# Kernel optimization log

Measured on AMD Instinct MI355X. Metric: run time of the kernel, lower is better.

Reference implementation:

```python
import jax, jax.numpy as jnp
import numpy as np

B, C, H, W = 8, 512, 32, 32
MID = 64  # in_ch // k = 512 // 8
BN_EPS = 1e-5


def conv1x1(x, Wt, b):
    # x: [B,C,H,W], Wt: [O,C], b: [O]
    return jnp.einsum('bchw,oc->bohw', x, Wt) + b[None, :, None, None]


def batchnorm(x, gamma, beta):
    # train-mode BN: batch statistics over (B,H,W)
    mu = jnp.mean(x, axis=(0, 2, 3), keepdims=True)
    var = jnp.var(x, axis=(0, 2, 3), keepdims=True)
    xn = (x - mu) * jax.lax.rsqrt(var + BN_EPS)
    return xn * gamma[None, :, None, None] + beta[None, :, None, None]


def setup_inputs() -> dict:
    key = jax.random.key(0)
    ks = jax.random.split(key, 8)
    scale = 1.0 / np.sqrt(C)
    x = jax.random.normal(ks[0], (B, C, H, W), dtype=jnp.float32)
    Wf = jax.random.normal(ks[1], (MID, C), dtype=jnp.float32) * scale
    Wg = jax.random.normal(ks[2], (MID, C), dtype=jnp.float32) * scale
    Wh = jax.random.normal(ks[3], (MID, C), dtype=jnp.float32) * scale
    Wv = jax.random.normal(ks[4], (C, MID), dtype=jnp.float32) * (1.0 / np.sqrt(MID))
    return {
        'x': x,
        'Wf': Wf, 'bf': jnp.zeros((MID,), jnp.float32),
        'gamma_f': jnp.ones((MID,), jnp.float32), 'beta_f': jnp.zeros((MID,), jnp.float32),
        'Wg': Wg, 'bg': jnp.zeros((MID,), jnp.float32),
        'gamma_g': jnp.ones((MID,), jnp.float32), 'beta_g': jnp.zeros((MID,), jnp.float32),
        'Wh': Wh, 'bh': jnp.zeros((MID,), jnp.float32),
        'Wv': Wv, 'bv': jnp.zeros((C,), jnp.float32),
    }


def reference(x, Wf, bf, gamma_f, beta_f, Wg, bg, gamma_g, beta_g, Wh, bh, Wv, bv):
    b, c, h, w = x.shape
    hw = h * w
    f_x = jax.nn.relu(batchnorm(conv1x1(x, Wf, bf), gamma_f, beta_f)).reshape(b, MID, hw)
    g_x = jax.nn.relu(batchnorm(conv1x1(x, Wg, bg), gamma_g, beta_g)).reshape(b, MID, hw)
    h_x = conv1x1(x, Wh, bh).reshape(b, MID, hw)
    # z = f_x^T @ g_x : [B, HW, HW]
    z = jnp.einsum('bcn,bcm->bnm', f_x, g_x)
    # spectral normalization by the top singular value
    S = jnp.linalg.svd(z, compute_uv=False)  # sorted descending
    sigma = S[:, 0][:, None, None]
    attn = z / sigma
    # attn @ h_x^T -> [B, HW, MID], then permute to [B, MID, H, W]
    z2 = jnp.einsum('bnm,bcm->bcn', attn, h_x).reshape(b, MID, h, w)
    return conv1x1(z2, Wv, bv) + x
```

## Files before the change

### kernel.cpp

```cpp
#include <hip/hip_runtime.h>

#define B_   8
#define C_   512
#define HW_  1024
#define NCOL (B_*HW_)
#define NROWS 192
#define EPS  1e-5f
#define NCHUNK 32

#define YOFF   0
#define YSZ    (NROWS*NCOL)
#define SPOFF  (YOFF+YSZ)
#define SPSZ   256
#define WOFF   (SPOFF+SPSZ)
#define WSZ    98304
#define CPOFF  (WOFF+WSZ)
#define CPSZ   (24*NCHUNK*4096)
#define CMOFF  (CPOFF+CPSZ)
#define CMSZ   (24*4096)
#define ISOFF  (CMOFF+CMSZ)
#define UOFF   (ISOFF+16)

typedef unsigned short u16;
typedef __attribute__((ext_vector_type(8))) short short8;
typedef __attribute__((ext_vector_type(4))) float f32x4;

__device__ __forceinline__ u16 f2bf(float f) {
  unsigned u = __float_as_uint(f);
  unsigned r = u + 0x7fffu + ((u >> 16) & 1u);
  return (u16)(r >> 16);
}
__device__ __forceinline__ float bf2f(u16 h) {
  return __uint_as_float(((unsigned)h) << 16);
}
#define MFMA_B16(a,b,c) __builtin_amdgcn_mfma_f32_16x16x32_bf16(a,b,c,0,0,0)

#define FMA16(a, bb) \
  acc[0][0]+=a.x*bb.x; acc[0][1]+=a.x*bb.y; acc[0][2]+=a.x*bb.z; acc[0][3]+=a.x*bb.w; \
  acc[1][0]+=a.y*bb.x; acc[1][1]+=a.y*bb.y; acc[1][2]+=a.y*bb.z; acc[1][3]+=a.y*bb.w; \
  acc[2][0]+=a.z*bb.x; acc[2][1]+=a.z*bb.y; acc[2][2]+=a.z*bb.z; acc[2][3]+=a.z*bb.w; \
  acc[3][0]+=a.w*bb.x; acc[3][1]+=a.w*bb.y; acc[3][2]+=a.w*bb.z; acc[3][3]+=a.w*bb.w;

__global__ __launch_bounds__(256) void k_prep(
    const float* __restrict__ Wf, const float* __restrict__ Wg,
    const float* __restrict__ Wh, float* __restrict__ ws)
{
  u16* Whi = (u16*)(ws + WOFF);
  u16* Wlo = Whi + NROWS*C_;
  const int e4 = blockIdx.x*256 + threadIdx.x;
  const int e  = e4*4;
  const int row = e >> 9, k = e & 511;
  const float* src = (row < 64) ? &Wf[row*C_ + k]
                   : (row < 128) ? &Wg[(row-64)*C_ + k]
                   : &Wh[(row-128)*C_ + k];
  const float4 v = *reinterpret_cast<const float4*>(src);
  u16 h0=f2bf(v.x), h1=f2bf(v.y), h2=f2bf(v.z), h3=f2bf(v.w);
  u16 l0=f2bf(v.x-bf2f(h0)), l1=f2bf(v.y-bf2f(h1)), l2=f2bf(v.z-bf2f(h2)), l3=f2bf(v.w-bf2f(h3));
  uint2 ph; ph.x = (unsigned)h0 | ((unsigned)h1<<16); ph.y = (unsigned)h2 | ((unsigned)h3<<16);
  uint2 pl; pl.x = (unsigned)l0 | ((unsigned)l1<<16); pl.y = (unsigned)l2 | ((unsigned)l3<<16);
  *reinterpret_cast<uint2*>(&Whi[e]) = ph;
  *reinterpret_cast<uint2*>(&Wlo[e]) = pl;
}

__global__ __launch_bounds__(256) void k_conv(
    const float* __restrict__ x,
    const float* __restrict__ bf, const float* __restrict__ bg, const float* __restrict__ bh,
    float* __restrict__ ws)
{
  __shared__ u16 Xh[8*32*8];
  __shared__ u16 Xl[8*32*8];
  __shared__ u16 Swh[4][3][2][512];
  __shared__ u16 Swl[4][3][2][512];
  const u16* Whi = (const u16*)(ws + WOFF);
  const u16* Wlo = Whi + NROWS*C_;
  const int bid = blockIdx.x;
  const int n0  = bid * 32;
  const int b   = n0 >> 10;
  const int hw0 = n0 & 1023;
  const int t   = threadIdx.x;
  const int lane = t & 63;
  const int wid  = t >> 6;
  const int wrow0 = wid * 48;
  const int cst = t & 31, kg2 = t >> 5;
  const int lm = lane & 15, lk = lane >> 4;

  float xr[64];
  {
    const float* xp = x + ((size_t)(b*C_ + kg2*8))*HW_ + hw0 + cst;
    #pragma unroll
    for (int j = 0; j < 8; ++j)
      #pragma unroll
      for (int i = 0; i < 8; ++i)
        xr[j*8+i] = xp[(size_t)(j*64 + i)*HW_];
  }

  f32x4 acc[3][2];
  #pragma unroll
  for (int i=0;i<3;++i) { acc[i][0]=(f32x4)0.f; acc[i][1]=(f32x4)0.f; }

  #pragma unroll
  for (int j = 0; j < 8; ++j) {
    const int kk = j*64;
    __syncthreads();
    {
      uint4 th[6], tl[6];
      #pragma unroll
      for (int mt = 0; mt < 3; ++mt)
        #pragma unroll
        for (int kb = 0; kb < 2; ++kb) {
          const size_t widx = (size_t)(wrow0 + mt*16 + lm)*C_ + kk + kb*32 + lk*8;
          th[mt*2+kb] = *reinterpret_cast<const uint4*>(&Whi[widx]);
          tl[mt*2+kb] = *reinterpret_cast<const uint4*>(&Wlo[widx]);
        }
      #pragma unroll
      for (int mt = 0; mt < 3; ++mt)
        #pragma unroll
        for (int kb = 0; kb < 2; ++kb) {
          *reinterpret_cast<uint4*>(&Swh[wid][mt][kb][lane*8]) = th[mt*2+kb];
          *reinterpret_cast<uint4*>(&Swl[wid][mt][kb][lane*8]) = tl[mt*2+kb];
        }
    }
    {
      u16 hb[8], lb[8];
      #pragma unroll
      for (int i=0;i<8;++i) {
        const float v = xr[j*8+i];
        hb[i] = f2bf(v); lb[i] = f2bf(v - bf2f(hb[i]));
      }
      uint4 ph, pl;
      ph.x=(unsigned)hb[0]|((unsigned)hb[1]<<16); ph.y=(unsigned)hb[2]|((unsigned)hb[3]<<16);
      ph.z=(unsigned)hb[4]|((unsigned)hb[5]<<16); ph.w=(unsigned)hb[6]|((unsigned)hb[7]<<16);
      pl.x=(unsigned)lb[0]|((unsigned)lb[1]<<16); pl.y=(unsigned)lb[2]|((unsigned)lb[3]<<16);
      pl.z=(unsigned)lb[4]|((unsigned)lb[5]<<16); pl.w=(unsigned)lb[6]|((unsigned)lb[7]<<16);
      *reinterpret_cast<uint4*>(&Xh[(kg2*32+cst)*8]) = ph;
      *reinterpret_cast<uint4*>(&Xl[(kg2*32+cst)*8]) = pl;
    }
    __syncthreads();
    #pragma unroll
    for (int kb = 0; kb < 2; ++kb) {
      short8 bhf[2], blf[2];
      #pragma unroll
      for (int nt = 0; nt < 2; ++nt) {
        const int col = nt*16 + lm;
        const int idx = ((kb*4 + lk)*32 + col)*8;
        bhf[nt] = *reinterpret_cast<const short8*>(&Xh[idx]);
        blf[nt] = *reinterpret_cast<const short8*>(&Xl[idx]);
      }
      #pragma unroll
      for (int mt = 0; mt < 3; ++mt) {
        const short8 ah = *reinterpret_cast<const short8*>(&Swh[wid][mt][kb][lane*8]);
        const short8 al = *reinterpret_cast<const short8*>(&Swl[wid][mt][kb][lane*8]);
        #pragma unroll
        for (int nt = 0; nt < 2; ++nt) {
          acc[mt][nt] = MFMA_B16(ah, bhf[nt], acc[mt][nt]);
          acc[mt][nt] = MFMA_B16(al, bhf[nt], acc[mt][nt]);
          acc[mt][nt] = MFMA_B16(ah, blf[nt], acc[mt][nt]);
        }
      }
    }
  }
  #pragma unroll
  for (int mt = 0; mt < 3; ++mt) {
    const int rbase = wrow0 + mt*16;
    const float* bp = (rbase < 64) ? bf : (rbase < 128) ? bg : bh;
    const int rloc0 = (rbase & 63) + lk*4;
    #pragma unroll
    for (int nt = 0; nt < 2; ++nt) {
      const int col = n0 + nt*16 + lm;
      #pragma unroll
      for (int r = 0; r < 4; ++r) {
        const int row = rbase + lk*4 + r;
        ws[YOFF + (size_t)row*NCOL + col] = acc[mt][nt][r] + bp[rloc0 + r];
      }
    }
  }
}

__global__ __launch_bounds__(256) void k_stats(float* __restrict__ ws)
{
  const int r = blockIdx.x;
  const float4* Yr = reinterpret_cast<const float4*>(ws + YOFF + (size_t)r*NCOL);
  const int t = threadIdx.x;
  float s = 0.f, s2 = 0.f;
  for (int n = t; n < NCOL/4; n += 256) {
    const float4 v = Yr[n];
    s  += (v.x+v.y)+(v.z+v.w);
    s2 += (v.x*v.x+v.y*v.y)+(v.z*v.z+v.w*v.w);
  }
  __shared__ float sh[256], sh2[256];
  sh[t] = s; sh2[t] = s2;
  __syncthreads();
  for (int st = 128; st > 0; st >>= 1) {
    if (t < st) { sh[t] += sh[t+st]; sh2[t] += sh2[t+st]; }
    __syncthreads();
  }
  if (t == 0) {
    ws[SPOFF + r*2 + 0] = sh[0];
    ws[SPOFF + r*2 + 1] = sh2[0];
  }
}

__global__ __launch_bounds__(256) void k_cpart(
    const float* __restrict__ gamma_f, const float* __restrict__ beta_f,
    const float* __restrict__ gamma_g, const float* __restrict__ beta_g,
    float* __restrict__ ws)
{
  __shared__ u16 Sh[3][64][40];
  __shared__ u16 Sl[3][64][40];
  __shared__ float scs[128], sfs[128];
  const int chunk = blockIdx.x, b = blockIdx.y;
  const int t = threadIdx.x;
  if (t < 128) {
    const float s  = ws[SPOFF + t*2 + 0];
    const float s2 = ws[SPOFF + t*2 + 1];
    const float mean = s*(1.0f/NCOL);
    const float var  = s2*(1.0f/NCOL) - mean*mean;
    const float g  = (t < 64) ? gamma_f[t] : gamma_g[t-64];
    const float be = (t < 64) ? beta_f[t]  : beta_g[t-64];
    const float sc = g * rsqrtf(var + EPS);
    scs[t] = sc; sfs[t] = be - mean*sc;
  }
  __syncthreads();
  const int bcol0 = b*1024 + chunk*32;
  for (int q = t; q < 1536; q += 256) {
    const int mm = q >> 9, rem = q & 511;
    const int r = rem >> 3, c4 = (rem & 7) * 4;
    const float4 v = *reinterpret_cast<const float4*>(
        &ws[YOFF + (size_t)(mm*64 + r)*NCOL + bcol0 + c4]);
    float v0, v1, v2, v3;
    if (mm < 2) {
      const float sc = scs[mm*64 + r], sf = sfs[mm*64 + r];
      v0 = fmaxf(sc*v.x+sf, 0.f); v1 = fmaxf(sc*v.y+sf, 0.f);
      v2 = fmaxf(sc*v.z+sf, 0.f); v3 = fmaxf(sc*v.w+sf, 0.f);
    } else { v0=v.x; v1=v.y; v2=v.z; v3=v.w; }
    const u16 h0=f2bf(v0), h1=f2bf(v1), h2=f2bf(v2), h3=f2bf(v3);
    uint2 ph; ph.x=(unsigned)h0|((unsigned)h1<<16); ph.y=(unsigned)h2|((unsigned)h3<<16);
    uint2 pl;
    pl.x=(unsigned)f2bf(v0-bf2f(h0)) | ((unsigned)f2bf(v1-bf2f(h1))<<16);
    pl.y=(unsigned)f2bf(v2-bf2f(h2)) | ((unsigned)f2bf(v3-bf2f(h3))<<16);
    *reinterpret_cast<uint2*>(&Sh[mm][r][c4]) = ph;
    *reinterpret_cast<uint2*>(&Sl[mm][r][c4]) = pl;
  }
  __syncthreads();
  {
    const int lane = t & 63, wid = t >> 6;
    const int lm = lane & 15, lk = lane >> 4;
    const int mt0 = (wid >> 1)*2, nt0 = (wid & 1)*2;
    const int ko = lk*8;
    short8 ah[3][2], al[3][2];
    #pragma unroll
    for (int m = 0; m < 3; ++m)
      #pragma unroll
      for (int mi = 0; mi < 2; ++mi) {
        const int row = (mt0+mi)*16 + lm;
        ah[m][mi] = *reinterpret_cast<const short8*>(&Sh[m][row][ko]);
        al[m][mi] = *reinterpret_cast<const short8*>(&Sl[m][row][ko]);
      }
    short8 bhf[2][2], blf[2][2];
    #pragma unroll
    for (int m = 0; m < 2; ++m)
      #pragma unroll
      for (int ni = 0; ni < 2; ++ni) {
        const int row = (nt0+ni)*16 + lm;
        bhf[m][ni] = *reinterpret_cast<const short8*>(&Sh[m][row][ko]);
        blf[m][ni] = *reinterpret_cast<const short8*>(&Sl[m][row][ko]);
      }
    f32x4 acc2[3][2][2];
    #pragma unroll
    for (int p=0;p<3;++p) for (int i=0;i<2;++i) for (int j=0;j<2;++j) acc2[p][i][j]=(f32x4)0.f;
    #pragma unroll
    for (int p = 0; p < 3; ++p) {
      const int am = p;
      const int bm = (p==0) ? 0 : 1;
      #pragma unroll
      for (int mi = 0; mi < 2; ++mi)
        #pragma unroll
        for (int ni = 0; ni < 2; ++ni) {
          acc2[p][mi][ni] = MFMA_B16(ah[am][mi], bhf[bm][ni], acc2[p][mi][ni]);
          acc2[p][mi][ni] = MFMA_B16(al[am][mi], bhf[bm][ni], acc2[p][mi][ni]);
          acc2[p][mi][ni] = MFMA_B16(ah[am][mi], blf[bm][ni], acc2[p][mi][ni]);
        }
    }
    float* cp = ws + CPOFF;
    #pragma unroll
    for (int p = 0; p < 3; ++p) {
      float* base = cp + ((size_t)((b*3+p)*NCHUNK + chunk))*4096;
      #pragma unroll
      for (int mi = 0; mi < 2; ++mi)
        #pragma unroll
        for (int ni = 0; ni < 2; ++ni) {
          const int col = (nt0+ni)*16 + lm;
          #pragma unroll
          for (int r = 0; r < 4; ++r) {
            const int row = (mt0+mi)*16 + lk*4 + r;
            base[(size_t)row*64 + col] = acc2[p][mi][ni][r];
          }
        }
    }
  }
}

__global__ __launch_bounds__(256) void k_creduce(float* __restrict__ ws)
{
  const int m = blockIdx.y;
  const int q = blockIdx.x*256 + threadIdx.x;
  const float4* src = reinterpret_cast<const float4*>(ws + CPOFF) + (size_t)m*NCHUNK*1024;
  float4 s = {0.f,0.f,0.f,0.f};
  #pragma unroll 8
  for (int ch = 0; ch < NCHUNK; ++ch) {
    const float4 p = src[(size_t)ch*1024 + q];
    s.x+=p.x; s.y+=p.y; s.z+=p.z; s.w+=p.w;
  }
  *(reinterpret_cast<float4*>(ws + CMOFF) + (size_t)m*1024 + q) = s;
}

__global__ __launch_bounds__(256) void k_su(const float* __restrict__ Wv, float* __restrict__ ws)
{
  __shared__ float smA[64][64];
  __shared__ float smB[64][64];
  const int bid = blockIdx.x;
  const int t = threadIdx.x;
  if (bid < 64) {
    const int b = bid >> 3, rt = bid & 7;
    const float* T = ws + CMOFF + (size_t)(b*3+2)*4096;
    for (int q = t; q < 1024; q += 256)
      *(reinterpret_cast<float4*>(&smB[0][0]) + q) = *(reinterpret_cast<const float4*>(T) + q);
    for (int q = t; q < 1024; q += 256) {
      const int row = q >> 4;
      const int c4  = (q & 15) * 4;
      const float4 wv = *reinterpret_cast<const float4*>(&Wv[(size_t)(rt*64+row)*64 + c4]);
      smA[c4+0][row]=wv.x; smA[c4+1][row]=wv.y; smA[c4+2][row]=wv.z; smA[c4+3][row]=wv.w;
    }
    __syncthreads();
    const int ti = t >> 4, tj = t & 15;
    float acc[4][4] = {};
    #pragma unroll
    for (int c = 0; c < 64; ++c) {
      const float4 a  = *reinterpret_cast<const float4*>(&smA[c][ti*4]);
      const float4 bb = *reinterpret_cast<const float4*>(&smB[c][tj*4]);
      FMA16(a, bb)
    }
    #pragma unroll
    for (int i = 0; i < 4; ++i) {
      float4 o; o.x = acc[i][0]; o.y = acc[i][1]; o.z = acc[i][2]; o.w = acc[i][3];
      *reinterpret_cast<float4*>(&ws[UOFF + ((size_t)b*512 + rt*64 + ti*4+i)*64 + tj*4]) = o;
    }
  } else {
    const int b = bid - 64;
    float* vsh = &smA[0][0];
    float* ush = &smA[1][0];
    const float* Cf = ws + CMOFF + (size_t)(b*3+0)*4096;
    const float* Cg = ws + CMOFF + (size_t)(b*3+1)*4096;
    float cfr[64], cgr[64];
    if (t < 64) {
      #pragma unroll
      for (int k4 = 0; k4 < 16; ++k4) {
        const float4 fa = *reinterpret_cast<const float4*>(&Cf[t*64 + k4*4]);
        const float4 fc = *reinterpret_cast<const float4*>(&Cg[t*64 + k4*4]);
        cfr[k4*4+0]=fa.x; cfr[k4*4+1]=fa.y; cfr[k4*4+2]=fa.z; cfr[k4*4+3]=fa.w;
        cgr[k4*4+0]=fc.x; cgr[k4*4+1]=fc.y; cgr[k4*4+2]=fc.z; cgr[k4*4+3]=fc.w;
      }
    }
    float vloc = 0.125f;
    if (t < 64) vsh[t] = vloc;
    __syncthreads();
    const int NIT = 16;
    float lambda = 0.f;
    for (int it = 0; it <= NIT; ++it) {
      if (t < 64) {
        float u0=0.f,u1=0.f,u2=0.f,u3=0.f;
        #pragma unroll
        for (int j4 = 0; j4 < 16; ++j4) {
          const float4 vq = *reinterpret_cast<const float4*>(&vsh[j4*4]);
          u0 += cfr[j4*4+0]*vq.x; u1 += cfr[j4*4+1]*vq.y;
          u2 += cfr[j4*4+2]*vq.z; u3 += cfr[j4*4+3]*vq.w;
        }
        ush[t] = (u0+u1)+(u2+u3);
      }
      __syncthreads();
      float w = 0.f;
      if (t < 64) {
        float w0=0.f,w1=0.f,w2=0.f,w3=0.f;
        #pragma unroll
        for (int j4 = 0; j4 < 16; ++j4) {
          const float4 uq = *reinterpret_cast<const float4*>(&ush[j4*4]);
          w0 += cgr[j4*4+0]*uq.x; w1 += cgr[j4*4+1]*uq.y;
          w2 += cgr[j4*4+2]*uq.z; w3 += cgr[j4*4+3]*uq.w;
        }
        w = (w0+w1)+(w2+w3);
      }
      if (it == NIT) {
        if (t < 64) {
          float num = vloc * w;
          #pragma unroll
          for (int off = 32; off > 0; off >>= 1) num += __shfl_xor(num, off);
          lambda = num;
        }
      } else {
        if (t < 64) {
          float n2 = w*w;
          #pragma unroll
          for (int off = 32; off > 0; off >>= 1) n2 += __shfl_xor(n2, off);
          const float rn = rsqrtf(fmaxf(n2, 1e-30f));
          vloc = w * rn;
        }
        __syncthreads();
        if (t < 64) vsh[t] = vloc;
        __syncthreads();
      }
    }
    if (t == 0) ws[ISOFF + b] = rsqrtf(fmaxf(lambda, 1e-30f));
  }
}

__global__ __launch_bounds__(256) void k_final(
    const float* __restrict__ x, const float* __restrict__ bv,
    const float* __restrict__ gamma_f, const float* __restrict__ beta_f,
    float* __restrict__ out, const float* __restrict__ ws)
{
  __shared__ float Ut[64][64];
  __shared__ float Fl[64][64];
  __shared__ float scF[64], sfF[64];
  const int nt = blockIdx.x, ot = blockIdx.y, b = blockIdx.z;
  const int t = threadIdx.x;
  if (t < 64) {
    const float s  = ws[SPOFF + t*2 + 0];
    const float s2 = ws[SPOFF + t*2 + 1];
    const float mean = s*(1.0f/NCOL);
    const float var  = s2*(1.0f/NCOL) - mean*mean;
    const float sc = gamma_f[t] * rsqrtf(var + EPS);
    scF[t] = sc; sfF[t] = beta_f[t] - mean*sc;
  }
  for (int q = t; q < 1024; q += 256) {
    const int row = q >> 4, k4 = (q & 15)*4;
    const float4 uv = *reinterpret_cast<const float4*>(
        &ws[UOFF + ((size_t)b*512 + ot*64 + row)*64 + k4]);
    Ut[k4+0][row]=uv.x; Ut[k4+1][row]=uv.y; Ut[k4+2][row]=uv.z; Ut[k4+3][row]=uv.w;
  }
  for (int q = t; q < 1024; q += 256) {
    const int k = q >> 4, c4 = (q & 15)*4;
    const float4 yv = *reinterpret_cast<const float4*>(
        &ws[YOFF + (size_t)k*NCOL + b*1024 + nt*64 + c4]);
    Fl[k][c4+0]=yv.x; Fl[k][c4+1]=yv.y; Fl[k][c4+2]=yv.z; Fl[k][c4+3]=yv.w;
  }
  __syncthreads();
  for (int q = t; q < 1024; q += 256) {
    const int k = q >> 4, c4 = (q & 15)*4;
    const float s = scF[k], f = sfF[k];
    Fl[k][c4+0]=fmaxf(s*Fl[k][c4+0]+f,0.f); Fl[k][c4+1]=fmaxf(s*Fl[k][c4+1]+f,0.f);
    Fl[k][c4+2]=fmaxf(s*Fl[k][c4+2]+f,0.f); Fl[k][c4+3]=fmaxf(s*Fl[k][c4+3]+f,0.f);
  }
  __syncthreads();
  const float isig = ws[ISOFF + b];
  const int ti = t >> 4, tj = t & 15;
  float acc[4][4] = {};
  #pragma unroll
  for (int k = 0; k < 64; ++k) {
    const float4 a  = *reinterpret_cast<const float4*>(&Ut[k][ti*4]);
    const float4 bb = *reinterpret_cast<const float4*>(&Fl[k][tj*4]);
    FMA16(a, bb)
  }
  #pragma unroll
  for (int i = 0; i < 4; ++i) {
    const int oc = ot*64 + ti*4 + i;
    const float bvv = bv[oc];
    const size_t base = ((size_t)b*C_ + oc)*HW_ + nt*64 + tj*4;
    const float4 xv = *reinterpret_cast<const float4*>(&x[base]);
    float4 o;
    o.x = acc[i][0]*isig+bvv+xv.x; o.y = acc[i][1]*isig+bvv+xv.y;
    o.z = acc[i][2]*isig+bvv+xv.z; o.w = acc[i][3]*isig+bvv+xv.w;
    *reinterpret_cast<float4*>(&out[base]) = o;
  }
}

extern "C" void kernel_launch(void* const* d_in, const int* in_sizes, int n_in,
                              void* d_out, int out_size, void* d_ws, size_t ws_size,
                              hipStream_t stream) {
  (void)in_sizes; (void)n_in; (void)out_size; (void)ws_size;
  const float* x       = (const float*)d_in[0];
  const float* Wf      = (const float*)d_in[1];
  const float* bf      = (const float*)d_in[2];
  const float* gamma_f = (const float*)d_in[3];
  const float* beta_f  = (const float*)d_in[4];
  const float* Wg      = (const float*)d_in[5];
  const float* bg      = (const float*)d_in[6];
  const float* gamma_g = (const float*)d_in[7];
  const float* beta_g  = (const float*)d_in[8];
  const float* Wh      = (const float*)d_in[9];
  const float* bh      = (const float*)d_in[10];
  const float* Wv      = (const float*)d_in[11];
  const float* bv      = (const float*)d_in[12];
  float* out = (float*)d_out;
  float* ws  = (float*)d_ws;

  k_prep   <<<96,             256, 0, stream>>>(Wf, Wg, Wh, ws);
  k_conv   <<<256,            256, 0, stream>>>(x, bf, bg, bh, ws);
  k_stats  <<<128,            256, 0, stream>>>(ws);
  k_cpart  <<<dim3(NCHUNK,8), 256, 0, stream>>>(gamma_f, beta_f, gamma_g, beta_g, ws);
  k_creduce<<<dim3(4,24),     256, 0, stream>>>(ws);
  k_su     <<<72,             256, 0, stream>>>(Wv, ws);
  k_final  <<<dim3(16,8,8),   256, 0, stream>>>(x, bv, gamma_f, beta_f, out, ws);
}
```

Measured before the change: 77.75 us.

## Fuse stats, cpart, creduce and su kernels into one persistent kernel with grid barriers

Merges four middle kernels into a single 256-block kernel that uses a hierarchical atomic grid barrier between phases, with a shared-memory union for the per-phase buffers. The stats phase is split into half-rows so that all 256 blocks take part, and later readers sum the two partial values. This removes three kernel launches and their inter-kernel gaps, at the cost of spin-wait barrier overhead and a requirement that all 256 blocks be co-resident. The barrier counters are zeroed in k_prep on every call.

```diff
diff --git a/kernel.cpp b/kernel.cpp
--- a/kernel.cpp
+++ b/kernel.cpp
@@ -7,11 +7,12 @@
 #define NROWS 192
 #define EPS  1e-5f
 #define NCHUNK 32
+#define NBLK 256
 
 #define YOFF   0
 #define YSZ    (NROWS*NCOL)
 #define SPOFF  (YOFF+YSZ)
-#define SPSZ   256
+#define SPSZ   512
 #define WOFF   (SPOFF+SPSZ)
 #define WSZ    98304
 #define CPOFF  (WOFF+WSZ)
@@ -20,6 +21,8 @@
 #define CMSZ   (24*4096)
 #define ISOFF  (CMOFF+CMSZ)
 #define UOFF   (ISOFF+16)
+#define USZ    (B_*512*64)
+#define BAROFF (UOFF+USZ)
 
 typedef unsigned short u16;
 typedef __attribute__((ext_vector_type(8))) short short8;
@@ -41,10 +44,39 @@
   acc[2][0]+=a.z*bb.x; acc[2][1]+=a.z*bb.y; acc[2][2]+=a.z*bb.z; acc[2][3]+=a.z*bb.w; \
   acc[3][0]+=a.w*bb.x; acc[3][1]+=a.w*bb.y; acc[3][2]+=a.w*bb.z; acc[3][3]+=a.w*bb.w;
 
+__device__ __forceinline__ void gbar2(unsigned* base, int phase) {
+  __syncthreads();
+  if (threadIdx.x == 0) {
+    const int g = blockIdx.x & 7;
+    unsigned* lc  = base + g*32;
+    unsigned* gc  = base + 256;
+    unsigned* rel = base + 288 + g*32;
+    __builtin_amdgcn_fence(__ATOMIC_RELEASE, "agent");
+    const unsigned my = __hip_atomic_fetch_add(lc, 1u, __ATOMIC_ACQ_REL, __HIP_MEMORY_SCOPE_AGENT);
+    if (my == (unsigned)(phase+1)*(NBLK/8) - 1u) {
+      const unsigned gg = __hip_atomic_fetch_add(gc, 1u, __ATOMIC_ACQ_REL, __HIP_MEMORY_SCOPE_AGENT);
+      if (gg == (unsigned)(phase+1)*8u - 1u) {
+        #pragma unroll
+        for (int k = 0; k < 8; ++k)
+          __hip_atomic_store(base + 288 + k*32, (unsigned)(phase+1),
+                             __ATOMIC_RELEASE, __HIP_MEMORY_SCOPE_AGENT);
+      }
+    }
+    while (__hip_atomic_load(rel, __ATOMIC_ACQUIRE, __HIP_MEMORY_SCOPE_AGENT) < (unsigned)(phase+1))
+      __builtin_amdgcn_s_sleep(1);
+  }
+  __syncthreads();
+  __builtin_amdgcn_fence(__ATOMIC_ACQUIRE, "agent");
+}
+
 __global__ __launch_bounds__(256) void k_prep(
     const float* __restrict__ Wf, const float* __restrict__ Wg,
     const float* __restrict__ Wh, float* __restrict__ ws)
 {
+  if (blockIdx.x == 0) {
+    unsigned* bw = reinterpret_cast<unsigned*>(ws + BAROFF);
+    for (int i = threadIdx.x; i < 1024; i += 256) bw[i] = 0u;
+  }
   u16* Whi = (u16*)(ws + WOFF);
   u16* Wlo = Whi + NROWS*C_;
   const int e4 = blockIdx.x*256 + threadIdx.x;
@@ -176,168 +208,174 @@
   }
 }
 
-__global__ __launch_bounds__(256) void k_stats(float* __restrict__ ws)
-{
-  const int r = blockIdx.x;
-  const float4* Yr = reinterpret_cast<const float4*>(ws + YOFF + (size_t)r*NCOL);
-  const int t = threadIdx.x;
-  float s = 0.f, s2 = 0.f;
-  for (int n = t; n < NCOL/4; n += 256) {
-    const float4 v = Yr[n];
-    s  += (v.x+v.y)+(v.z+v.w);
-    s2 += (v.x*v.x+v.y*v.y)+(v.z*v.z+v.w*v.w);
-  }
-  __shared__ float sh[256], sh2[256];
-  sh[t] = s; sh2[t] = s2;
-  __syncthreads();
-  for (int st = 128; st > 0; st >>= 1) {
-    if (t < st) { sh[t] += sh[t+st]; sh2[t] += sh2[t+st]; }
-    __syncthreads();
-  }
-  if (t == 0) {
-    ws[SPOFF + r*2 + 0] = sh[0];
-    ws[SPOFF + r*2 + 1] = sh2[0];
-  }
-}
-
-__global__ __launch_bounds__(256) void k_cpart(
+union alignas(16) MidSm {
+  struct { float sh[256]; float sh2[256]; } stats;
+  struct { u16 Sh[3][64][40]; u16 Sl[3][64][40]; float scs[128]; float sfs[128]; } cpart;
+  struct { float A[64][64]; float B[64][64]; } su;
+};
+
+__global__ __launch_bounds__(256) void k_mid(
     const float* __restrict__ gamma_f, const float* __restrict__ beta_f,
     const float* __restrict__ gamma_g, const float* __restrict__ beta_g,
-    float* __restrict__ ws)
+    const float* __restrict__ Wv, float* __restrict__ ws)
 {
-  __shared__ u16 Sh[3][64][40];
-  __shared__ u16 Sl[3][64][40];
-  __shared__ float scs[128], sfs[128];
-  const int chunk = blockIdx.x, b = blockIdx.y;
-  const int t = threadIdx.x;
-  if (t < 128) {
-    const float s  = ws[SPOFF + t*2 + 0];
-    const float s2 = ws[SPOFF + t*2 + 1];
-    const float mean = s*(1.0f/NCOL);
-    const float var  = s2*(1.0f/NCOL) - mean*mean;
-    const float g  = (t < 64) ? gamma_f[t] : gamma_g[t-64];
-    const float be = (t < 64) ? beta_f[t]  : beta_g[t-64];
-    const float sc = g * rsqrtf(var + EPS);
-    scs[t] = sc; sfs[t] = be - mean*sc;
-  }
-  __syncthreads();
-  const int bcol0 = b*1024 + chunk*32;
-  for (int q = t; q < 1536; q += 256) {
-    const int mm = q >> 9, rem = q & 511;
-    const int r = rem >> 3, c4 = (rem & 7) * 4;
-    const float4 v = *reinterpret_cast<const float4*>(
-        &ws[YOFF + (size_t)(mm*64 + r)*NCOL + bcol0 + c4]);
-    float v0, v1, v2, v3;
-    if (mm < 2) {
-      const float sc = scs[mm*64 + r], sf = sfs[mm*64 + r];
-      v0 = fmaxf(sc*v.x+sf, 0.f); v1 = fmaxf(sc*v.y+sf, 0.f);
-      v2 = fmaxf(sc*v.z+sf, 0.f); v3 = fmaxf(sc*v.w+sf, 0.f);
-    } else { v0=v.x; v1=v.y; v2=v.z; v3=v.w; }
-    const u16 h0=f2bf(v0), h1=f2bf(v1), h2=f2bf(v2), h3=f2bf(v3);
-    uint2 ph; ph.x=(unsigned)h0|((unsigned)h1<<16); ph.y=(unsigned)h2|((unsigned)h3<<16);
-    uint2 pl;
-    pl.x=(unsigned)f2bf(v0-bf2f(h0)) | ((unsigned)f2bf(v1-bf2f(h1))<<16);
-    pl.y=(unsigned)f2bf(v2-bf2f(h2)) | ((unsigned)f2bf(v3-bf2f(h3))<<16);
-    *reinterpret_cast<uint2*>(&Sh[mm][r][c4]) = ph;
-    *reinterpret_cast<uint2*>(&Sl[mm][r][c4]) = pl;
-  }
-  __syncthreads();
-  {
-    const int lane = t & 63, wid = t >> 6;
-    const int lm = lane & 15, lk = lane >> 4;
-    const int mt0 = (wid >> 1)*2, nt0 = (wid & 1)*2;
-    const int ko = lk*8;
-    short8 ah[3][2], al[3][2];
-    #pragma unroll
-    for (int m = 0; m < 3; ++m)
-      #pragma unroll
-      for (int mi = 0; mi < 2; ++mi) {
-        const int row = (mt0+mi)*16 + lm;
-        ah[m][mi] = *reinterpret_cast<const short8*>(&Sh[m][row][ko]);
-        al[m][mi] = *reinterpret_cast<const short8*>(&Sl[m][row][ko]);
-      }
-    short8 bhf[2][2], blf[2][2];
-    #pragma unroll
-    for (int m = 0; m < 2; ++m)
-      #pragma unroll
-      for (int ni = 0; ni < 2; ++ni) {
-        const int row = (nt0+ni)*16 + lm;
-        bhf[m][ni] = *reinterpret_cast<const short8*>(&Sh[m][row][ko]);
-        blf[m][ni] = *reinterpret_cast<const short8*>(&Sl[m][row][ko]);
-      }
-    f32x4 acc2[3][2][2];
-    #pragma unroll
-    for (int p=0;p<3;++p) for (int i=0;i<2;++i) for (int j=0;j<2;++j) acc2[p][i][j]=(f32x4)0.f;
-    #pragma unroll
-    for (int p = 0; p < 3; ++p) {
-      const int am = p;
-      const int bm = (p==0) ? 0 : 1;
-      #pragma unroll
-      for (int mi = 0; mi < 2; ++mi)
-        #pragma unroll
-        for (int ni = 0; ni < 2; ++ni) {
-          acc2[p][mi][ni] = MFMA_B16(ah[am][mi], bhf[bm][ni], acc2[p][mi][ni]);
-          acc2[p][mi][ni] = MFMA_B16(al[am][mi], bhf[bm][ni], acc2[p][mi][ni]);
-          acc2[p][mi][ni] = MFMA_B16(ah[am][mi], blf[bm][ni], acc2[p][mi][ni]);
-        }
-    }
-    float* cp = ws + CPOFF;
-    #pragma unroll
-    for (int p = 0; p < 3; ++p) {
-      float* base = cp + ((size_t)((b*3+p)*NCHUNK + chunk))*4096;
-      #pragma unroll
-      for (int mi = 0; mi < 2; ++mi)
-        #pragma unroll
-        for (int ni = 0; ni < 2; ++ni) {
-          const int col = (nt0+ni)*16 + lm;
-          #pragma unroll
-          for (int r = 0; r < 4; ++r) {
-            const int row = (mt0+mi)*16 + lk*4 + r;
-            base[(size_t)row*64 + col] = acc2[p][mi][ni][r];
-          }
-        }
-    }
-  }
-}
-
-__global__ __launch_bounds__(256) void k_creduce(float* __restrict__ ws)
-{
-  const int m = blockIdx.y;
-  const int q = blockIdx.x*256 + threadIdx.x;
-  const float4* src = reinterpret_cast<const float4*>(ws + CPOFF) + (size_t)m*NCHUNK*1024;
-  float4 s = {0.f,0.f,0.f,0.f};
-  #pragma unroll 8
-  for (int ch = 0; ch < NCHUNK; ++ch) {
-    const float4 p = src[(size_t)ch*1024 + q];
-    s.x+=p.x; s.y+=p.y; s.z+=p.z; s.w+=p.w;
-  }
-  *(reinterpret_cast<float4*>(ws + CMOFF) + (size_t)m*1024 + q) = s;
-}
-
-__global__ __launch_bounds__(256) void k_su(const float* __restrict__ Wv, float* __restrict__ ws)
-{
-  __shared__ float smA[64][64];
-  __shared__ float smB[64][64];
+  __shared__ MidSm sm;
   const int bid = blockIdx.x;
   const int t = threadIdx.x;
+  unsigned* bar = reinterpret_cast<unsigned*>(ws + BAROFF);
+
+  {
+    const int row = bid >> 1, half = bid & 1;
+    const float4* Yr = reinterpret_cast<const float4*>(ws + YOFF + (size_t)row*NCOL + half*4096);
+    float s = 0.f, s2 = 0.f;
+    for (int q = t; q < 1024; q += 256) {
+      const float4 v = Yr[q];
+      s  += (v.x+v.y)+(v.z+v.w);
+      s2 += (v.x*v.x+v.y*v.y)+(v.z*v.z+v.w*v.w);
+    }
+    sm.stats.sh[t] = s; sm.stats.sh2[t] = s2;
+    __syncthreads();
+    for (int st = 128; st > 0; st >>= 1) {
+      if (t < st) { sm.stats.sh[t] += sm.stats.sh[t+st]; sm.stats.sh2[t] += sm.stats.sh2[t+st]; }
+      __syncthreads();
+    }
+    if (t == 0) {
+      ws[SPOFF + row*4 + half*2 + 0] = sm.stats.sh[0];
+      ws[SPOFF + row*4 + half*2 + 1] = sm.stats.sh2[0];
+    }
+  }
+  gbar2(bar, 0);
+
+  {
+    const int chunk = bid & 31, b = bid >> 5;
+    if (t < 128) {
+      const float* sp = ws + SPOFF;
+      const float s  = sp[t*4+0] + sp[t*4+2];
+      const float s2 = sp[t*4+1] + sp[t*4+3];
+      const float mean = s*(1.0f/NCOL);
+      const float var  = s2*(1.0f/NCOL) - mean*mean;
+      const float g  = (t < 64) ? gamma_f[t] : gamma_g[t-64];
+      const float be = (t < 64) ? beta_f[t]  : beta_g[t-64];
+      const float sc = g * rsqrtf(var + EPS);
+      sm.cpart.scs[t] = sc; sm.cpart.sfs[t] = be - mean*sc;
+    }
+    __syncthreads();
+    const int bcol0 = b*1024 + chunk*32;
+    for (int q = t; q < 1536; q += 256) {
+      const int mm = q >> 9, rem = q & 511;
+      const int r = rem >> 3, c4 = (rem & 7) * 4;
+      const float4 v = *reinterpret_cast<const float4*>(
+          &ws[YOFF + (size_t)(mm*64 + r)*NCOL + bcol0 + c4]);
+      float v0, v1, v2, v3;
+      if (mm < 2) {
+        const float sc = sm.cpart.scs[mm*64 + r], sf = sm.cpart.sfs[mm*64 + r];
+        v0 = fmaxf(sc*v.x+sf, 0.f); v1 = fmaxf(sc*v.y+sf, 0.f);
+        v2 = fmaxf(sc*v.z+sf, 0.f); v3 = fmaxf(sc*v.w+sf, 0.f);
+      } else { v0=v.x; v1=v.y; v2=v.z; v3=v.w; }
+      const u16 h0=f2bf(v0), h1=f2bf(v1), h2=f2bf(v2), h3=f2bf(v3);
+      uint2 ph; ph.x=(unsigned)h0|((unsigned)h1<<16); ph.y=(unsigned)h2|((unsigned)h3<<16);
+      uint2 pl;
+      pl.x=(unsigned)f2bf(v0-bf2f(h0)) | ((unsigned)f2bf(v1-bf2f(h1))<<16);
+      pl.y=(unsigned)f2bf(v2-bf2f(h2)) | ((unsigned)f2bf(v3-bf2f(h3))<<16);
+      *reinterpret_cast<uint2*>(&sm.cpart.Sh[mm][r][c4]) = ph;
+      *reinterpret_cast<uint2*>(&sm.cpart.Sl[mm][r][c4]) = pl;
+    }
+    __syncthreads();
+    {
+      const int lane = t & 63, wid = t >> 6;
+      const int lm = lane & 15, lk = lane >> 4;
+      const int mt0 = (wid >> 1)*2, nt0 = (wid & 1)*2;
+      const int ko = lk*8;
+      short8 ah[3][2], al[3][2];
+      #pragma unroll
+      for (int m = 0; m < 3; ++m)
+        #pragma unroll
+        for (int mi = 0; mi < 2; ++mi) {
+          const int row = (mt0+mi)*16 + lm;
+          ah[m][mi] = *reinterpret_cast<const short8*>(&sm.cpart.Sh[m][row][ko]);
+          al[m][mi] = *reinterpret_cast<const short8*>(&sm.cpart.Sl[m][row][ko]);
+        }
+      short8 bhf[2][2], blf[2][2];
+      #pragma unroll
+      for (int m = 0; m < 2; ++m)
+        #pragma unroll
+        for (int ni = 0; ni < 2; ++ni) {
+          const int row = (nt0+ni)*16 + lm;
+          bhf[m][ni] = *reinterpret_cast<const short8*>(&sm.cpart.Sh[m][row][ko]);
+          blf[m][ni] = *reinterpret_cast<const short8*>(&sm.cpart.Sl[m][row][ko]);
+        }
+      f32x4 acc2[3][2][2];
+      #pragma unroll
+      for (int p=0;p<3;++p) for (int i=0;i<2;++i) for (int j=0;j<2;++j) acc2[p][i][j]=(f32x4)0.f;
+      #pragma unroll
+      for (int p = 0; p < 3; ++p) {
+        const int am = p;
+        const int bm = (p==0) ? 0 : 1;
+        #pragma unroll
+        for (int mi = 0; mi < 2; ++mi)
+          #pragma unroll
+          for (int ni = 0; ni < 2; ++ni) {
+            acc2[p][mi][ni] = MFMA_B16(ah[am][mi], bhf[bm][ni], acc2[p][mi][ni]);
+            acc2[p][mi][ni] = MFMA_B16(al[am][mi], bhf[bm][ni], acc2[p][mi][ni]);
+            acc2[p][mi][ni] = MFMA_B16(ah[am][mi], blf[bm][ni], acc2[p][mi][ni]);
+          }
+      }
+      float* cp = ws + CPOFF;
+      #pragma unroll
+      for (int p = 0; p < 3; ++p) {
+        float* base = cp + ((size_t)((b*3+p)*NCHUNK + chunk))*4096;
+        #pragma unroll
+        for (int mi = 0; mi < 2; ++mi)
+          #pragma unroll
+          for (int ni = 0; ni < 2; ++ni) {
+            const int col = (nt0+ni)*16 + lm;
+            #pragma unroll
+            for (int r = 0; r < 4; ++r) {
+              const int row = (mt0+mi)*16 + lk*4 + r;
+              base[(size_t)row*64 + col] = acc2[p][mi][ni][r];
+            }
+          }
+      }
+    }
+  }
+  gbar2(bar, 1);
+
+  {
+    const float4* cp4 = reinterpret_cast<const float4*>(ws + CPOFF);
+    float4* cm4 = reinterpret_cast<float4*>(ws + CMOFF);
+    const unsigned idx = (unsigned)bid*256 + t;
+    if (idx < 24u*1024u) {
+      const unsigned m = idx >> 10, q = idx & 1023u;
+      const float4* src = cp4 + (size_t)m*NCHUNK*1024 + q;
+      float4 s = {0.f,0.f,0.f,0.f};
+      #pragma unroll 8
+      for (int ch = 0; ch < NCHUNK; ++ch) {
+        const float4 p = src[(size_t)ch*1024];
+        s.x+=p.x; s.y+=p.y; s.z+=p.z; s.w+=p.w;
+      }
+      cm4[(size_t)m*1024 + q] = s;
+    }
+  }
+  gbar2(bar, 2);
+
   if (bid < 64) {
     const int b = bid >> 3, rt = bid & 7;
     const float* T = ws + CMOFF + (size_t)(b*3+2)*4096;
     for (int q = t; q < 1024; q += 256)
-      *(reinterpret_cast<float4*>(&smB[0][0]) + q) = *(reinterpret_cast<const float4*>(T) + q);
+      *(reinterpret_cast<float4*>(&sm.su.B[0][0]) + q) = *(reinterpret_cast<const float4*>(T) + q);
     for (int q = t; q < 1024; q += 256) {
       const int row = q >> 4;
       const int c4  = (q & 15) * 4;
       const float4 wv = *reinterpret_cast<const float4*>(&Wv[(size_t)(rt*64+row)*64 + c4]);
-      smA[c4+0][row]=wv.x; smA[c4+1][row]=wv.y; smA[c4+2][row]=wv.z; smA[c4+3][row]=wv.w;
+      sm.su.A[c4+0][row]=wv.x; sm.su.A[c4+1][row]=wv.y; sm.su.A[c4+2][row]=wv.z; sm.su.A[c4+3][row]=wv.w;
     }
     __syncthreads();
     const int ti = t >> 4, tj = t & 15;
     float acc[4][4] = {};
     #pragma unroll
     for (int c = 0; c < 64; ++c) {
-      const float4 a  = *reinterpret_cast<const float4*>(&smA[c][ti*4]);
-      const float4 bb = *reinterpret_cast<const float4*>(&smB[c][tj*4]);
+      const float4 a  = *reinterpret_cast<const float4*>(&sm.su.A[c][ti*4]);
+      const float4 bb = *reinterpret_cast<const float4*>(&sm.su.B[c][tj*4]);
       FMA16(a, bb)
     }
     #pragma unroll
@@ -345,10 +383,10 @@
       float4 o; o.x = acc[i][0]; o.y = acc[i][1]; o.z = acc[i][2]; o.w = acc[i][3];
       *reinterpret_cast<float4*>(&ws[UOFF + ((size_t)b*512 + rt*64 + ti*4+i)*64 + tj*4]) = o;
     }
-  } else {
+  } else if (bid < 72) {
     const int b = bid - 64;
-    float* vsh = &smA[0][0];
-    float* ush = &smA[1][0];
+    float* vsh = &sm.su.A[0][0];
+    float* ush = &sm.su.A[1][0];
     const float* Cf = ws + CMOFF + (size_t)(b*3+0)*4096;
     const float* Cg = ws + CMOFF + (size_t)(b*3+1)*4096;
     float cfr[64], cgr[64];
@@ -424,8 +462,9 @@
   const int nt = blockIdx.x, ot = blockIdx.y, b = blockIdx.z;
   const int t = threadIdx.x;
   if (t < 64) {
-    const float s  = ws[SPOFF + t*2 + 0];
-    const float s2 = ws[SPOFF + t*2 + 1];
+    const float* sp = ws + SPOFF;
+    const float s  = sp[t*4+0] + sp[t*4+2];
+    const float s2 = sp[t*4+1] + sp[t*4+3];
     const float mean = s*(1.0f/NCOL);
     const float var  = s2*(1.0f/NCOL) - mean*mean;
     const float sc = gamma_f[t] * rsqrtf(var + EPS);
@@ -493,11 +532,8 @@
   float* out = (float*)d_out;
   float* ws  = (float*)d_ws;
 
-  k_prep   <<<96,             256, 0, stream>>>(Wf, Wg, Wh, ws);
-  k_conv   <<<256,            256, 0, stream>>>(x, bf, bg, bh, ws);
-  k_stats  <<<128,            256, 0, stream>>>(ws);
-  k_cpart  <<<dim3(NCHUNK,8), 256, 0, stream>>>(gamma_f, beta_f, gamma_g, beta_g, ws);
-  k_creduce<<<dim3(4,24),     256, 0, stream>>>(ws);
-  k_su     <<<72,             256, 0, stream>>>(Wv, ws);
-  k_final  <<<dim3(16,8,8),   256, 0, stream>>>(x, bv, gamma_f, beta_f, out, ws);
-}
+  k_prep <<<96,            256, 0, stream>>>(Wf, Wg, Wh, ws);
+  k_conv <<<256,           256, 0, stream>>>(x, bf, bg, bh, ws);
+  k_mid  <<<NBLK,          256, 0, stream>>>(gamma_f, beta_f, gamma_g, beta_g, Wv, ws);
+  k_final<<<dim3(16,8,8),  256, 0, stream>>>(x, bv, gamma_f, beta_f, out, ws);
+}
```

Result: slower. 208.0 us (+167.6%).
